# Optimization experiments

Hardware: AMD Instinct MI355X
Metric: run time of the kernel (lower is better)

Reference implementation:

```python
import jax, jax.numpy as jnp
import numpy as np
from jax import lax

B, L, S, D = 2, 8, 512, 256


def setup_inputs() -> dict:
    key = jax.random.key(0)
    ks = jax.random.split(key, 12)
    s = 1.0 / np.sqrt(D)
    return {
        "features": jax.random.normal(ks[0], (B, L, S, D), jnp.float32),
        "source_features": jax.random.normal(ks[1], (B, S, D), jnp.float32),
        "target_features": jax.random.normal(ks[2], (B, S, D), jnp.float32),
        # GRU params (torch layout: [3D, D] with gate order r, z, n)
        "W_ih": jax.random.uniform(ks[3], (3 * D, D), jnp.float32, -s, s),
        "W_hh": jax.random.uniform(ks[4], (3 * D, D), jnp.float32, -s, s),
        "b_ih": jax.random.uniform(ks[5], (3 * D,), jnp.float32, -s, s),
        "b_hh": jax.random.uniform(ks[6], (3 * D,), jnp.float32, -s, s),
        # causal_predictor: Linear(2D, D) -> ReLU -> Linear(D, D) -> Sigmoid
        "W1": jax.random.uniform(ks[7], (D, 2 * D), jnp.float32, -s, s),
        "b1": jax.random.uniform(ks[8], (D,), jnp.float32, -s, s),
        "W2": jax.random.uniform(ks[9], (D, D), jnp.float32, -s, s),
        "b2": jax.random.uniform(ks[10], (D,), jnp.float32, -s, s),
    }


def _gru(x, W_ih, W_hh, b_ih, b_hh):
    # x: [N, T, D] batch-first; returns all hidden states [N, T, D]
    N, T, d = x.shape
    gx = jnp.einsum('ntd,gd->ntg', x, W_ih) + b_ih  # [N, T, 3D]

    def step(h, gx_t):
        gh = h @ W_hh.T + b_hh
        r = jax.nn.sigmoid(gx_t[:, :d] + gh[:, :d])
        z = jax.nn.sigmoid(gx_t[:, d:2 * d] + gh[:, d:2 * d])
        n = jnp.tanh(gx_t[:, 2 * d:] + r * gh[:, 2 * d:])
        h_new = (1.0 - z) * n + z * h
        return h_new, h_new

    h0 = jnp.zeros((N, d), x.dtype)
    _, outs = lax.scan(step, h0, jnp.swapaxes(gx, 0, 1))  # [T, N, D]
    return jnp.swapaxes(outs, 0, 1)


def reference(features, source_features, target_features,
              W_ih, W_hh, b_ih, b_hh, W1, b1, W2, b2):
    b, l, s, d = features.shape
    fdim = jnp.float32(d)

    # --- track_feature_evolution, vectorized over seq positions ---
    # per-position GRU over the layer axis == one GRU over a B*S batch
    x = jnp.transpose(features, (0, 2, 1, 3)).reshape(b * s, l, d)
    evolution_out = _gru(x, W_ih, W_hh, b_ih, b_hh).reshape(b, s, l, d)

    prev = features[:, :-1]            # [B, L-1, S, D]
    nxt = features[:, 1:]
    eps = jnp.float32(1e-8)
    na = jnp.maximum(jnp.linalg.norm(prev, axis=-1), eps)
    nb = jnp.maximum(jnp.linalg.norm(nxt, axis=-1), eps)
    stability = (jnp.sum(prev * nxt, axis=-1) / (na * nb)).mean(axis=0)  # [L-1, S]

    act = jnp.sum((features > 0.1).astype(jnp.float32), axis=-1)  # [B, L, S]
    emergence = (act[:, 1:] - act[:, :-1]).mean(axis=0) / fdim    # [L-1, S]
    decay = (act[:, :-1] - act[:, 1:]).mean(axis=0) / fdim        # [L-1, S]

    # --- compute_causal_strength ---
    # combined[b,s,i,:D] = source[b,s,:]; combined[b,s,i,D+k] = target[b,s,i] (all k)
    # first Linear(2D->D) therefore splits into:  source @ W1a^T  +  target_i * sum_k W1b[:,k]
    W1a = W1[:, :d]                     # [D, D]
    wb = jnp.sum(W1[:, d:], axis=1)     # [D]
    A = jnp.einsum('bsd,od->bso', source_features, W1a) + b1  # [B, S, D]
    h = A[:, :, None, :] + target_features[:, :, :, None] * wb  # [B, S, D(i), D(o)]
    h = jax.nn.relu(h)
    out2 = jax.nn.sigmoid(jnp.einsum('bsio,po->bsip', h, W2) + b2)  # [B, S, D, D]
    causal_matrix = out2.mean(axis=(0, 1))  # [D, D]

    return stability, emergence, decay, causal_matrix, evolution_out
```

## Files before the change

kernel.cpp:

```cpp
#include <hip/hip_runtime.h>
#include <hip/hip_bf16.h>
#include <stdint.h>

typedef unsigned short u16;
typedef __bf16 v8bf __attribute__((ext_vector_type(8)));
typedef float f32x4 __attribute__((ext_vector_type(4)));

#define WS_WB    0u
#define WS_WIHB  4096u
#define WS_WHHB  397312u
#define WS_W2B   790528u
#define WS_A     921600u
#define WS_GX    2097152u
#define WS_PART  27262976u

#define OUT_STAB   0
#define OUT_EMER   3584
#define OUT_DECAY  7168
#define OUT_CAUSAL 10752
#define OUT_EVO    76288

__device__ __forceinline__ u16 f2bfu(float f){
    union { float f; uint32_t u; } v; v.f = f;
    uint32_t u = v.u;
    return (u16)((u + 0x7fffu + ((u >> 16) & 1u)) >> 16);
}
__device__ __forceinline__ float sigmoidf_fast(float x){
    float e = __builtin_amdgcn_exp2f(-1.4426950408889634f * x);
    return __builtin_amdgcn_rcpf(1.0f + e);
}
__device__ __forceinline__ float tanhf_fast(float x){
    float e = __builtin_amdgcn_exp2f(-2.8853900817779268f * x);
    return __builtin_amdgcn_rcpf(1.0f + e) * 2.0f - 1.0f;
}
__device__ __forceinline__ f32x4 mfma16(v8bf a, v8bf b, f32x4 c){
    return __builtin_amdgcn_mfma_f32_16x16x32_bf16(a, b, c, 0, 0, 0);
}
__device__ __forceinline__ v8bf cvt8(const float* p){
    float4 a = *(const float4*)p;
    float4 b = *(const float4*)(p + 4);
    v8bf r;
    r[0] = (__bf16)a.x; r[1] = (__bf16)a.y; r[2] = (__bf16)a.z; r[3] = (__bf16)a.w;
    r[4] = (__bf16)b.x; r[5] = (__bf16)b.y; r[6] = (__bf16)b.z; r[7] = (__bf16)b.w;
    return r;
}

__global__ void k_prep(const float* __restrict__ Wih, const float* __restrict__ Whh,
                       const float* __restrict__ W2,  const float* __restrict__ W1,
                       u16* __restrict__ wihb, u16* __restrict__ whhb,
                       u16* __restrict__ w2b, float* __restrict__ wb){
    int idx = blockIdx.x * 256 + threadIdx.x;
    if (idx < 196608) {
        wihb[idx] = f2bfu(Wih[idx]);
    } else if (idx < 393216) {
        int i = idx - 196608; whhb[i] = f2bfu(Whh[i]);
    } else if (idx < 458752) {
        int i = idx - 393216; w2b[i] = f2bfu(W2[i]);
    } else if (idx < 459008) {
        int o = idx - 458752;
        float s = 0.f;
        const float4* p = (const float4*)&W1[o * 512 + 256];
        for (int j = 0; j < 64; j++){
            float4 v = p[j];
            s += v.x + v.y + v.z + v.w;
        }
        wb[o] = s;
    }
}

__global__ __launch_bounds__(256) void k_Agemm(
        const float* __restrict__ src, const float* __restrict__ W1,
        const float* __restrict__ b1, float* __restrict__ A){
    const int bs0 = blockIdx.x * 16;
    const int tid = threadIdx.x, lane = tid & 63, w = tid >> 6;
    const int l15 = lane & 15, quad = lane >> 4;

    v8bf xa[8];
    for (int k = 0; k < 8; k++)
        xa[k] = cvt8(&src[(bs0 + l15) * 256 + k * 32 + quad * 8]);

    f32x4 acc[4];
    for (int nt = 0; nt < 4; nt++) acc[nt] = (f32x4){0.f, 0.f, 0.f, 0.f};
    for (int k = 0; k < 8; k++){
        int d0 = k * 32 + quad * 8;
        for (int nt = 0; nt < 4; nt++){
            int o = w * 64 + nt * 16 + l15;
            v8bf bfr = cvt8(&W1[o * 512 + d0]);
            acc[nt] = mfma16(xa[k], bfr, acc[nt]);
        }
    }
    for (int nt = 0; nt < 4; nt++){
        int o = w * 64 + nt * 16 + l15;
        float bb = b1[o];
        for (int r = 0; r < 4; r++)
            A[(bs0 + quad * 4 + r) * 256 + o] = acc[nt][r] + bb;
    }
}

__global__ void k_metrics(const float* __restrict__ feat, float* __restrict__ out){
    const int bid = blockIdx.x;
    const int l = bid >> 9, s = bid & 511;
    const int lane = threadIdx.x;
    float stab = 0.f, emer = 0.f;
    for (int b = 0; b < 2; b++){
        const float* p = feat + ((size_t)((b * 8 + l) * 512 + s)) * 256;
        const float* n = feat + ((size_t)((b * 8 + l + 1) * 512 + s)) * 256;
        float4 pv = *(const float4*)(p + lane * 4);
        float4 nv = *(const float4*)(n + lane * 4);
        float dot = pv.x * nv.x + pv.y * nv.y + pv.z * nv.z + pv.w * nv.w;
        float na2 = pv.x * pv.x + pv.y * pv.y + pv.z * pv.z + pv.w * pv.w;
        float nb2 = nv.x * nv.x + nv.y * nv.y + nv.z * nv.z + nv.w * nv.w;
        float ap = ((pv.x > 0.1f) ? 1.f : 0.f) + ((pv.y > 0.1f) ? 1.f : 0.f)
                 + ((pv.z > 0.1f) ? 1.f : 0.f) + ((pv.w > 0.1f) ? 1.f : 0.f);
        float an = ((nv.x > 0.1f) ? 1.f : 0.f) + ((nv.y > 0.1f) ? 1.f : 0.f)
                 + ((nv.z > 0.1f) ? 1.f : 0.f) + ((nv.w > 0.1f) ? 1.f : 0.f);
        for (int off = 32; off > 0; off >>= 1){
            dot += __shfl_xor(dot, off);
            na2 += __shfl_xor(na2, off);
            nb2 += __shfl_xor(nb2, off);
            ap  += __shfl_xor(ap,  off);
            an  += __shfl_xor(an,  off);
        }
        float na = fmaxf(__builtin_sqrtf(na2), 1e-8f);
        float nb = fmaxf(__builtin_sqrtf(nb2), 1e-8f);
        stab += dot / (na * nb);
        emer += (an - ap);
    }
    if (lane == 0){
        int o = l * 512 + s;
        float e = emer * 0.5f * (1.0f / 256.0f);
        out[OUT_STAB  + o] = stab * 0.5f;
        out[OUT_EMER  + o] = e;
        out[OUT_DECAY + o] = -e;
    }
}

__global__ __launch_bounds__(256, 2) void k_causal(
        const float* __restrict__ Aws, const float* __restrict__ wbws,
        const u16* __restrict__ w2b, const float* __restrict__ tgt,
        const float* __restrict__ b2, float* __restrict__ part){
    const int bid = blockIdx.x;
    const int chunk = bid >> 2, q = bid & 3;
    const int i0 = (q & 1) * 128, p0 = (q >> 1) * 128;
    const int tid = threadIdx.x, lane = tid & 63, w = tid >> 6;
    const int l15 = lane & 15, quad = lane >> 4;

    __shared__ u16  w2s[128 * 264];
    __shared__ float a_s[256];
    __shared__ float wb_s[256];
    __shared__ float t_s[128];

    {
        int r = tid >> 1, half = tid & 1;
        const uint4* gsrc = (const uint4*)&w2b[(p0 + r) * 256 + half * 128];
        uint4* ldst = (uint4*)&w2s[r * 264 + half * 128];
        for (int j = 0; j < 16; j++) ldst[j] = gsrc[j];
    }
    wb_s[tid] = wbws[tid];

    float bb[8];
    for (int nt = 0; nt < 8; nt++) bb[nt] = b2[p0 + nt * 16 + l15];

    f32x4 sig[2][8];
    for (int mt = 0; mt < 2; mt++) for (int nt = 0; nt < 8; nt++)
        sig[mt][nt] = (f32x4){0.f, 0.f, 0.f, 0.f};

    for (int ss = 0; ss < 8; ss++){
        const int bs = chunk * 8 + ss;
        __syncthreads();
        a_s[tid] = Aws[bs * 256 + tid];
        if (tid < 128) t_s[tid] = tgt[bs * 256 + i0 + tid];
        __syncthreads();

        float tv[2];
        for (int mt = 0; mt < 2; mt++) tv[mt] = t_s[w * 32 + mt * 16 + l15];

        f32x4 acc[2][8];
        for (int mt = 0; mt < 2; mt++) for (int nt = 0; nt < 8; nt++)
            acc[mt][nt] = (f32x4){0.f, 0.f, 0.f, 0.f};

        for (int k = 0; k < 8; k++){
            const int o0 = k * 32 + quad * 8;
            float4 a0 = *(const float4*)&a_s[o0];
            float4 a1 = *(const float4*)&a_s[o0 + 4];
            float4 w0 = *(const float4*)&wb_s[o0];
            float4 w1v = *(const float4*)&wb_s[o0 + 4];
            v8bf afr[2];
            for (int mt = 0; mt < 2; mt++){
                float t = tv[mt];
                float e0 = fmaxf(fmaf(t, w0.x,  a0.x), 0.f);
                float e1 = fmaxf(fmaf(t, w0.y,  a0.y), 0.f);
                float e2 = fmaxf(fmaf(t, w0.z,  a0.z), 0.f);
                float e3 = fmaxf(fmaf(t, w0.w,  a0.w), 0.f);
                float e4 = fmaxf(fmaf(t, w1v.x, a1.x), 0.f);
                float e5 = fmaxf(fmaf(t, w1v.y, a1.y), 0.f);
                float e6 = fmaxf(fmaf(t, w1v.z, a1.z), 0.f);
                float e7 = fmaxf(fmaf(t, w1v.w, a1.w), 0.f);
                v8bf af;
                af[0] = (__bf16)e0; af[1] = (__bf16)e1;
                af[2] = (__bf16)e2; af[3] = (__bf16)e3;
                af[4] = (__bf16)e4; af[5] = (__bf16)e5;
                af[6] = (__bf16)e6; af[7] = (__bf16)e7;
                afr[mt] = af;
            }
            for (int nt = 0; nt < 8; nt++){
                v8bf bfr = *(const v8bf*)&w2s[(nt * 16 + l15) * 264 + o0];
                acc[0][nt] = mfma16(afr[0], bfr, acc[0][nt]);
                acc[1][nt] = mfma16(afr[1], bfr, acc[1][nt]);
            }
        }
        for (int mt = 0; mt < 2; mt++)
            for (int nt = 0; nt < 8; nt++)
                for (int r = 0; r < 4; r++)
                    sig[mt][nt][r] += sigmoidf_fast(acc[mt][nt][r] + bb[nt]);
    }

    float* pp = part + (size_t)chunk * 65536;
    for (int mt = 0; mt < 2; mt++)
        for (int r = 0; r < 4; r++){
            int i = i0 + w * 32 + mt * 16 + quad * 4 + r;
            for (int nt = 0; nt < 8; nt++){
                int p = p0 + nt * 16 + l15;
                pp[i * 256 + p] = sig[mt][nt][r];
            }
        }
}

__global__ void k_creduce(const float* __restrict__ part, float* __restrict__ out){
    const int idx = blockIdx.x * 256 + threadIdx.x;
    float s = 0.f;
    for (int c = 0; c < 128; c++)
        s += part[(size_t)c * 65536 + idx];
    out[OUT_CAUSAL + idx] = s * (1.0f / 1024.0f);
}

__global__ __launch_bounds__(256) void k_gx(
        const float* __restrict__ feat, const u16* __restrict__ wihb,
        const float* __restrict__ bih, float* __restrict__ gxws){
    const int mb = blockIdx.x / 6, nb = blockIdx.x % 6;
    const int tid = threadIdx.x, lane = tid & 63, w = tid >> 6;
    const int l15 = lane & 15, quad = lane >> 4;

    __shared__ u16 blds[128 * 264];

    {
        int r = tid >> 1, half = tid & 1;
        const uint4* gsrc = (const uint4*)&wihb[(nb * 128 + r) * 256 + half * 128];
        uint4* ldst = (uint4*)&blds[r * 264 + half * 128];
        for (int j = 0; j < 16; j++) ldst[j] = gsrc[j];
    }

    v8bf af[2][8];
    for (int mt = 0; mt < 2; mt++){
        int r = mb * 128 + w * 32 + mt * 16 + l15;
        int n = r >> 3, t = r & 7;
        int b = n >> 9, s = n & 511;
        const float* xp = feat + ((size_t)((b * 8 + t) * 512 + s)) * 256;
        for (int kk = 0; kk < 8; kk++)
            af[mt][kk] = cvt8(xp + kk * 32 + quad * 8);
    }
    __syncthreads();

    f32x4 acc[2][8];
    for (int mt = 0; mt < 2; mt++) for (int nt = 0; nt < 8; nt++)
        acc[mt][nt] = (f32x4){0.f, 0.f, 0.f, 0.f};
    for (int kk = 0; kk < 8; kk++){
        int k0 = kk * 32 + quad * 8;
        for (int nt = 0; nt < 8; nt++){
            v8bf bf = *(const v8bf*)&blds[(nt * 16 + l15) * 264 + k0];
            acc[0][nt] = mfma16(af[0][kk], bf, acc[0][nt]);
            acc[1][nt] = mfma16(af[1][kk], bf, acc[1][nt]);
        }
    }
    for (int nt = 0; nt < 8; nt++){
        int g = nb * 128 + nt * 16 + l15;
        float bias = bih[g];
        for (int mt = 0; mt < 2; mt++)
            for (int rr = 0; rr < 4; rr++){
                int row = mb * 128 + w * 32 + mt * 16 + quad * 4 + rr;
                gxws[(size_t)row * 768 + g] = acc[mt][nt][rr] + bias;
            }
    }
}

__global__ __launch_bounds__(512) void k_gruseq(
        const float* __restrict__ gxws, const u16* __restrict__ whhb,
        const float* __restrict__ bhh, float* __restrict__ out){
    const int n0 = blockIdx.x * 16;
    const int tid = threadIdx.x, lane = tid & 63, wv = tid >> 6;
    const int l15 = lane & 15, quad = lane >> 4;
    const int g0 = wv * 96;

    __shared__ float h_lds[16 * 260];
    __shared__ float g_lds[16 * 776];

    v8bf wreg[3][8];
    for (int nt = 0; nt < 3; nt++)
        for (int k = 0; k < 8; k++)
            wreg[nt][k] = *(const v8bf*)&whhb[(g0 + nt * 16 + l15) * 256 + k * 32 + quad * 8];

    float bias[6];
    for (int nt = 0; nt < 6; nt++) bias[nt] = bhh[g0 + nt * 16 + l15];

    for (int e = tid; e < 16 * 260; e += 512) h_lds[e] = 0.f;

    const int seq = tid >> 5, d0 = (tid & 31) * 8;
    const float* gxbase = gxws + (size_t)(n0 + seq) * 8 * 768 + d0;
    float* evobase = out + OUT_EVO + (size_t)(n0 + seq) * 8 * 256 + d0;
    __syncthreads();

    for (int t = 0; t < 8; t++){
        v8bf ha[8];
        for (int k = 0; k < 8; k++)
            ha[k] = cvt8(&h_lds[l15 * 260 + k * 32 + quad * 8]);
        f32x4 acc[6];
        for (int nt = 0; nt < 6; nt++) acc[nt] = (f32x4){0.f, 0.f, 0.f, 0.f};
        for (int k = 0; k < 8; k++){
            int dk = k * 32 + quad * 8;
            acc[0] = mfma16(ha[k], wreg[0][k], acc[0]);
            acc[1] = mfma16(ha[k], wreg[1][k], acc[1]);
            acc[2] = mfma16(ha[k], wreg[2][k], acc[2]);
            for (int nt = 3; nt < 6; nt++){
                v8bf bf = *(const v8bf*)&whhb[(g0 + nt * 16 + l15) * 256 + dk];
                acc[nt] = mfma16(ha[k], bf, acc[nt]);
            }
        }
        for (int nt = 0; nt < 6; nt++){
            int g = g0 + nt * 16 + l15;
            for (int rr = 0; rr < 4; rr++)
                g_lds[(quad * 4 + rr) * 776 + g] = acc[nt][rr] + bias[nt];
        }
        const float* gxp = gxbase + (size_t)t * 768;
        float4 x0a = *(const float4*)(gxp);
        float4 x0b = *(const float4*)(gxp + 4);
        float4 x1a = *(const float4*)(gxp + 256);
        float4 x1b = *(const float4*)(gxp + 260);
        float4 x2a = *(const float4*)(gxp + 512);
        float4 x2b = *(const float4*)(gxp + 516);
        __syncthreads();
        {
            const float* gh = &g_lds[seq * 776];
            float* hp = &h_lds[seq * 260 + d0];
            float4 g0a = *(const float4*)&gh[d0];
            float4 g0b = *(const float4*)&gh[d0 + 4];
            float4 g1a = *(const float4*)&gh[256 + d0];
            float4 g1b = *(const float4*)&gh[260 + d0];
            float4 g2a = *(const float4*)&gh[512 + d0];
            float4 g2b = *(const float4*)&gh[516 + d0];
            float4 h0 = *(const float4*)hp;
            float4 h1 = *(const float4*)(hp + 4);
            float gxr[8] = {x0a.x, x0a.y, x0a.z, x0a.w, x0b.x, x0b.y, x0b.z, x0b.w};
            float gxz[8] = {x1a.x, x1a.y, x1a.z, x1a.w, x1b.x, x1b.y, x1b.z, x1b.w};
            float gxn[8] = {x2a.x, x2a.y, x2a.z, x2a.w, x2b.x, x2b.y, x2b.z, x2b.w};
            float ghr[8] = {g0a.x, g0a.y, g0a.z, g0a.w, g0b.x, g0b.y, g0b.z, g0b.w};
            float ghz[8] = {g1a.x, g1a.y, g1a.z, g1a.w, g1b.x, g1b.y, g1b.z, g1b.w};
            float ghn[8] = {g2a.x, g2a.y, g2a.z, g2a.w, g2b.x, g2b.y, g2b.z, g2b.w};
            float hold[8] = {h0.x, h0.y, h0.z, h0.w, h1.x, h1.y, h1.z, h1.w};
            float hn[8];
            #pragma unroll
            for (int j = 0; j < 8; j++){
                float r  = sigmoidf_fast(gxr[j] + ghr[j]);
                float z  = sigmoidf_fast(gxz[j] + ghz[j]);
                float nn = tanhf_fast(fmaf(r, ghn[j], gxn[j]));
                hn[j] = (1.f - z) * nn + z * hold[j];
            }
            float4 v0 = {hn[0], hn[1], hn[2], hn[3]};
            float4 v1 = {hn[4], hn[5], hn[6], hn[7]};
            *(float4*)hp       = v0;
            *(float4*)(hp + 4) = v1;
            float* ep = evobase + (size_t)t * 256;
            *(float4*)ep       = v0;
            *(float4*)(ep + 4) = v1;
        }
        __syncthreads();
    }
}

extern "C" void kernel_launch(void* const* d_in, const int* in_sizes, int n_in,
                              void* d_out, int out_size, void* d_ws, size_t ws_size,
                              hipStream_t stream){
    const float* feat = (const float*)d_in[0];
    const float* src  = (const float*)d_in[1];
    const float* tgt  = (const float*)d_in[2];
    const float* Wih  = (const float*)d_in[3];
    const float* Whh  = (const float*)d_in[4];
    const float* bih  = (const float*)d_in[5];
    const float* bhh  = (const float*)d_in[6];
    const float* W1   = (const float*)d_in[7];
    const float* b1   = (const float*)d_in[8];
    const float* W2   = (const float*)d_in[9];
    const float* b2   = (const float*)d_in[10];
    float* out = (float*)d_out;
    char* ws = (char*)d_ws;

    float* wb   = (float*)(ws + WS_WB);
    u16*   wihb = (u16*)(ws + WS_WIHB);
    u16*   whhb = (u16*)(ws + WS_WHHB);
    u16*   w2b  = (u16*)(ws + WS_W2B);
    float* Aws  = (float*)(ws + WS_A);
    float* gxws = (float*)(ws + WS_GX);
    float* part = (float*)(ws + WS_PART);

    k_prep   <<<1793, 256, 0, stream>>>(Wih, Whh, W2, W1, wihb, whhb, w2b, wb);
    k_gx     <<<384,  256, 0, stream>>>(feat, wihb, bih, gxws);
    k_Agemm  <<<64,   256, 0, stream>>>(src, W1, b1, Aws);
    k_metrics<<<3584,  64, 0, stream>>>(feat, out);
    k_causal <<<512,  256, 0, stream>>>(Aws, wb, w2b, tgt, b2, part);
    k_creduce<<<256,  256, 0, stream>>>(part, out);
    k_gruseq <<<64,   512, 0, stream>>>(gxws, whhb, bhh, out);
}
```

Baseline: 246.8 us.

## Consolidate launches into fused pre/final kernels and pre-convert features to bf16

Merges the A-GEMM, metrics and weight-prep kernels into one k_pre launch, which also converts the features tensor to bf16 in a workspace region that aliases the later partial-sum buffer. k_gx then reads bf16 features directly instead of converting on the fly. k_causal loads all 8 steps of A and target values into shared memory up front, removing two barriers per step, and reads wb from global memory. The causal reduction runs as extra blocks of the GRU sequence kernel so it can overlap with it. Together these cut the launch count from seven to four, at the cost of an extra full pass to write the bf16 copy of the features.

```diff
diff --git a/kernel.cpp b/kernel.cpp
--- a/kernel.cpp
+++ b/kernel.cpp
@@ -13,6 +13,7 @@
 #define WS_A     921600u
 #define WS_GX    2097152u
 #define WS_PART  27262976u
+#define WS_FEATB 27262976u
 
 #define OUT_STAB   0
 #define OUT_EMER   3584
@@ -45,93 +46,144 @@
     return r;
 }
 
-__global__ void k_prep(const float* __restrict__ Wih, const float* __restrict__ Whh,
-                       const float* __restrict__ W2,  const float* __restrict__ W1,
-                       u16* __restrict__ wihb, u16* __restrict__ whhb,
-                       u16* __restrict__ w2b, float* __restrict__ wb){
-    int idx = blockIdx.x * 256 + threadIdx.x;
-    if (idx < 196608) {
-        wihb[idx] = f2bfu(Wih[idx]);
-    } else if (idx < 393216) {
-        int i = idx - 196608; whhb[i] = f2bfu(Whh[i]);
-    } else if (idx < 458752) {
-        int i = idx - 393216; w2b[i] = f2bfu(W2[i]);
-    } else if (idx < 459008) {
-        int o = idx - 458752;
-        float s = 0.f;
-        const float4* p = (const float4*)&W1[o * 512 + 256];
-        for (int j = 0; j < 64; j++){
-            float4 v = p[j];
-            s += v.x + v.y + v.z + v.w;
-        }
-        wb[o] = s;
-    }
-}
-
-__global__ __launch_bounds__(256) void k_Agemm(
-        const float* __restrict__ src, const float* __restrict__ W1,
-        const float* __restrict__ b1, float* __restrict__ A){
-    const int bs0 = blockIdx.x * 16;
+__global__ __launch_bounds__(256) void k_pre(
+        const float* __restrict__ feat, const float* __restrict__ src,
+        const float* __restrict__ Wih,  const float* __restrict__ Whh,
+        const float* __restrict__ W1,   const float* __restrict__ b1,
+        const float* __restrict__ W2,
+        u16* __restrict__ wihb, u16* __restrict__ whhb, u16* __restrict__ w2b,
+        float* __restrict__ wb, u16* __restrict__ featb,
+        float* __restrict__ A, float* __restrict__ out){
+    const int bid = blockIdx.x, tid = threadIdx.x;
+    if (bid < 64){
+        const int bs0 = bid * 16;
+        const int lane = tid & 63, w = tid >> 6;
+        const int l15 = lane & 15, quad = lane >> 4;
+        v8bf xa[8];
+        for (int k = 0; k < 8; k++)
+            xa[k] = cvt8(&src[(bs0 + l15) * 256 + k * 32 + quad * 8]);
+        f32x4 acc[4];
+        for (int nt = 0; nt < 4; nt++) acc[nt] = (f32x4){0.f, 0.f, 0.f, 0.f};
+        for (int k = 0; k < 8; k++){
+            int d0 = k * 32 + quad * 8;
+            for (int nt = 0; nt < 4; nt++){
+                int o = w * 64 + nt * 16 + l15;
+                v8bf bfr = cvt8(&W1[o * 512 + d0]);
+                acc[nt] = mfma16(xa[k], bfr, acc[nt]);
+            }
+        }
+        for (int nt = 0; nt < 4; nt++){
+            int o = w * 64 + nt * 16 + l15;
+            float bb = b1[o];
+            for (int r = 0; r < 4; r++)
+                A[(bs0 + quad * 4 + r) * 256 + o] = acc[nt][r] + bb;
+        }
+    } else if (bid < 960){
+        const int pair = (bid - 64) * 4 + (tid >> 6);
+        const int l = pair >> 9, s = pair & 511;
+        const int lane = tid & 63;
+        float stab = 0.f, emer = 0.f;
+        for (int b = 0; b < 2; b++){
+            const float* p = feat + ((size_t)((b * 8 + l) * 512 + s)) * 256;
+            const float* n = feat + ((size_t)((b * 8 + l + 1) * 512 + s)) * 256;
+            float4 pv = *(const float4*)(p + lane * 4);
+            float4 nv = *(const float4*)(n + lane * 4);
+            float dot = pv.x * nv.x + pv.y * nv.y + pv.z * nv.z + pv.w * nv.w;
+            float na2 = pv.x * pv.x + pv.y * pv.y + pv.z * pv.z + pv.w * pv.w;
+            float nb2 = nv.x * nv.x + nv.y * nv.y + nv.z * nv.z + nv.w * nv.w;
+            float ap = ((pv.x > 0.1f) ? 1.f : 0.f) + ((pv.y > 0.1f) ? 1.f : 0.f)
+                     + ((pv.z > 0.1f) ? 1.f : 0.f) + ((pv.w > 0.1f) ? 1.f : 0.f);
+            float an = ((nv.x > 0.1f) ? 1.f : 0.f) + ((nv.y > 0.1f) ? 1.f : 0.f)
+                     + ((nv.z > 0.1f) ? 1.f : 0.f) + ((nv.w > 0.1f) ? 1.f : 0.f);
+            for (int off = 32; off > 0; off >>= 1){
+                dot += __shfl_xor(dot, off);
+                na2 += __shfl_xor(na2, off);
+                nb2 += __shfl_xor(nb2, off);
+                ap  += __shfl_xor(ap,  off);
+                an  += __shfl_xor(an,  off);
+            }
+            float na = fmaxf(__builtin_sqrtf(na2), 1e-8f);
+            float nb = fmaxf(__builtin_sqrtf(nb2), 1e-8f);
+            stab += dot / (na * nb);
+            emer += (an - ap);
+        }
+        if (lane == 0){
+            int o = l * 512 + s;
+            float e = emer * 0.5f * (1.0f / 256.0f);
+            out[OUT_STAB  + o] = stab * 0.5f;
+            out[OUT_EMER  + o] = e;
+            out[OUT_DECAY + o] = -e;
+        }
+    } else {
+        int idx = (bid - 960) * 256 + tid;
+        if (idx < 196608) {
+            wihb[idx] = f2bfu(Wih[idx]);
+        } else if (idx < 393216) {
+            int i = idx - 196608; whhb[i] = f2bfu(Whh[i]);
+        } else if (idx < 458752) {
+            int i = idx - 393216; w2b[i] = f2bfu(W2[i]);
+        } else if (idx < 459008) {
+            int o = idx - 458752;
+            float s = 0.f;
+            const float4* p = (const float4*)&W1[o * 512 + 256];
+            for (int j = 0; j < 64; j++){
+                float4 v = p[j];
+                s += v.x + v.y + v.z + v.w;
+            }
+            wb[o] = s;
+        } else {
+            int i = idx - 459008;
+            featb[i] = f2bfu(feat[i]);
+        }
+    }
+}
+
+__global__ __launch_bounds__(256) void k_gx(
+        const u16* __restrict__ featb, const u16* __restrict__ wihb,
+        const float* __restrict__ bih, float* __restrict__ gxws){
+    const int mb = blockIdx.x / 6, nb = blockIdx.x % 6;
     const int tid = threadIdx.x, lane = tid & 63, w = tid >> 6;
     const int l15 = lane & 15, quad = lane >> 4;
 
-    v8bf xa[8];
-    for (int k = 0; k < 8; k++)
-        xa[k] = cvt8(&src[(bs0 + l15) * 256 + k * 32 + quad * 8]);
-
-    f32x4 acc[4];
-    for (int nt = 0; nt < 4; nt++) acc[nt] = (f32x4){0.f, 0.f, 0.f, 0.f};
-    for (int k = 0; k < 8; k++){
-        int d0 = k * 32 + quad * 8;
-        for (int nt = 0; nt < 4; nt++){
-            int o = w * 64 + nt * 16 + l15;
-            v8bf bfr = cvt8(&W1[o * 512 + d0]);
-            acc[nt] = mfma16(xa[k], bfr, acc[nt]);
-        }
-    }
-    for (int nt = 0; nt < 4; nt++){
-        int o = w * 64 + nt * 16 + l15;
-        float bb = b1[o];
-        for (int r = 0; r < 4; r++)
-            A[(bs0 + quad * 4 + r) * 256 + o] = acc[nt][r] + bb;
-    }
-}
-
-__global__ void k_metrics(const float* __restrict__ feat, float* __restrict__ out){
-    const int bid = blockIdx.x;
-    const int l = bid >> 9, s = bid & 511;
-    const int lane = threadIdx.x;
-    float stab = 0.f, emer = 0.f;
-    for (int b = 0; b < 2; b++){
-        const float* p = feat + ((size_t)((b * 8 + l) * 512 + s)) * 256;
-        const float* n = feat + ((size_t)((b * 8 + l + 1) * 512 + s)) * 256;
-        float4 pv = *(const float4*)(p + lane * 4);
-        float4 nv = *(const float4*)(n + lane * 4);
-        float dot = pv.x * nv.x + pv.y * nv.y + pv.z * nv.z + pv.w * nv.w;
-        float na2 = pv.x * pv.x + pv.y * pv.y + pv.z * pv.z + pv.w * pv.w;
-        float nb2 = nv.x * nv.x + nv.y * nv.y + nv.z * nv.z + nv.w * nv.w;
-        float ap = ((pv.x > 0.1f) ? 1.f : 0.f) + ((pv.y > 0.1f) ? 1.f : 0.f)
-                 + ((pv.z > 0.1f) ? 1.f : 0.f) + ((pv.w > 0.1f) ? 1.f : 0.f);
-        float an = ((nv.x > 0.1f) ? 1.f : 0.f) + ((nv.y > 0.1f) ? 1.f : 0.f)
-                 + ((nv.z > 0.1f) ? 1.f : 0.f) + ((nv.w > 0.1f) ? 1.f : 0.f);
-        for (int off = 32; off > 0; off >>= 1){
-            dot += __shfl_xor(dot, off);
-            na2 += __shfl_xor(na2, off);
-            nb2 += __shfl_xor(nb2, off);
-            ap  += __shfl_xor(ap,  off);
-            an  += __shfl_xor(an,  off);
-        }
-        float na = fmaxf(__builtin_sqrtf(na2), 1e-8f);
-        float nb = fmaxf(__builtin_sqrtf(nb2), 1e-8f);
-        stab += dot / (na * nb);
-        emer += (an - ap);
-    }
-    if (lane == 0){
-        int o = l * 512 + s;
-        float e = emer * 0.5f * (1.0f / 256.0f);
-        out[OUT_STAB  + o] = stab * 0.5f;
-        out[OUT_EMER  + o] = e;
-        out[OUT_DECAY + o] = -e;
+    __shared__ u16 blds[128 * 264];
+
+    {
+        int r = tid >> 1, half = tid & 1;
+        const uint4* gsrc = (const uint4*)&wihb[(nb * 128 + r) * 256 + half * 128];
+        uint4* ldst = (uint4*)&blds[r * 264 + half * 128];
+        for (int j = 0; j < 16; j++) ldst[j] = gsrc[j];
+    }
+
+    v8bf af[2][8];
+    for (int mt = 0; mt < 2; mt++){
+        int r = mb * 128 + w * 32 + mt * 16 + l15;
+        int n = r >> 3, t = r & 7;
+        int b = n >> 9, s = n & 511;
+        const u16* xp = featb + ((size_t)((b * 8 + t) * 512 + s)) * 256;
+        for (int kk = 0; kk < 8; kk++)
+            af[mt][kk] = *(const v8bf*)(xp + kk * 32 + quad * 8);
+    }
+    __syncthreads();
+
+    f32x4 acc[2][8];
+    for (int mt = 0; mt < 2; mt++) for (int nt = 0; nt < 8; nt++)
+        acc[mt][nt] = (f32x4){0.f, 0.f, 0.f, 0.f};
+    for (int kk = 0; kk < 8; kk++){
+        int k0 = kk * 32 + quad * 8;
+        for (int nt = 0; nt < 8; nt++){
+            v8bf bf = *(const v8bf*)&blds[(nt * 16 + l15) * 264 + k0];
+            acc[0][nt] = mfma16(af[0][kk], bf, acc[0][nt]);
+            acc[1][nt] = mfma16(af[1][kk], bf, acc[1][nt]);
+        }
+    }
+    for (int nt = 0; nt < 8; nt++){
+        int g = nb * 128 + nt * 16 + l15;
+        float bias = bih[g];
+        for (int mt = 0; mt < 2; mt++)
+            for (int rr = 0; rr < 4; rr++){
+                int row = mb * 128 + w * 32 + mt * 16 + quad * 4 + rr;
+                gxws[(size_t)row * 768 + g] = acc[mt][nt][rr] + bias;
+            }
     }
 }
 
@@ -146,9 +198,8 @@
     const int l15 = lane & 15, quad = lane >> 4;
 
     __shared__ u16  w2s[128 * 264];
-    __shared__ float a_s[256];
-    __shared__ float wb_s[256];
-    __shared__ float t_s[128];
+    __shared__ float a_all[8 * 256];
+    __shared__ float t_all[8 * 128];
 
     {
         int r = tid >> 1, half = tid & 1;
@@ -156,7 +207,17 @@
         uint4* ldst = (uint4*)&w2s[r * 264 + half * 128];
         for (int j = 0; j < 16; j++) ldst[j] = gsrc[j];
     }
-    wb_s[tid] = wbws[tid];
+    {
+        const float4* src4 = (const float4*)&Aws[chunk * 8 * 256];
+        float4* dst4 = (float4*)a_all;
+        dst4[tid]       = src4[tid];
+        dst4[tid + 256] = src4[tid + 256];
+    }
+    {
+        int ss = tid >> 5, j4 = tid & 31;
+        float4 v = *(const float4*)&tgt[(chunk * 8 + ss) * 256 + i0 + j4 * 4];
+        *(float4*)&t_all[ss * 128 + j4 * 4] = v;
+    }
 
     float bb[8];
     for (int nt = 0; nt < 8; nt++) bb[nt] = b2[p0 + nt * 16 + l15];
@@ -165,15 +226,11 @@
     for (int mt = 0; mt < 2; mt++) for (int nt = 0; nt < 8; nt++)
         sig[mt][nt] = (f32x4){0.f, 0.f, 0.f, 0.f};
 
+    __syncthreads();
+
     for (int ss = 0; ss < 8; ss++){
-        const int bs = chunk * 8 + ss;
-        __syncthreads();
-        a_s[tid] = Aws[bs * 256 + tid];
-        if (tid < 128) t_s[tid] = tgt[bs * 256 + i0 + tid];
-        __syncthreads();
-
-        float tv[2];
-        for (int mt = 0; mt < 2; mt++) tv[mt] = t_s[w * 32 + mt * 16 + l15];
+        float tv0 = t_all[ss * 128 + w * 32 + l15];
+        float tv1 = t_all[ss * 128 + w * 32 + 16 + l15];
 
         f32x4 acc[2][8];
         for (int mt = 0; mt < 2; mt++) for (int nt = 0; nt < 8; nt++)
@@ -181,32 +238,37 @@
 
         for (int k = 0; k < 8; k++){
             const int o0 = k * 32 + quad * 8;
-            float4 a0 = *(const float4*)&a_s[o0];
-            float4 a1 = *(const float4*)&a_s[o0 + 4];
-            float4 w0 = *(const float4*)&wb_s[o0];
-            float4 w1v = *(const float4*)&wb_s[o0 + 4];
-            v8bf afr[2];
-            for (int mt = 0; mt < 2; mt++){
-                float t = tv[mt];
-                float e0 = fmaxf(fmaf(t, w0.x,  a0.x), 0.f);
-                float e1 = fmaxf(fmaf(t, w0.y,  a0.y), 0.f);
-                float e2 = fmaxf(fmaf(t, w0.z,  a0.z), 0.f);
-                float e3 = fmaxf(fmaf(t, w0.w,  a0.w), 0.f);
-                float e4 = fmaxf(fmaf(t, w1v.x, a1.x), 0.f);
-                float e5 = fmaxf(fmaf(t, w1v.y, a1.y), 0.f);
-                float e6 = fmaxf(fmaf(t, w1v.z, a1.z), 0.f);
-                float e7 = fmaxf(fmaf(t, w1v.w, a1.w), 0.f);
-                v8bf af;
-                af[0] = (__bf16)e0; af[1] = (__bf16)e1;
-                af[2] = (__bf16)e2; af[3] = (__bf16)e3;
-                af[4] = (__bf16)e4; af[5] = (__bf16)e5;
-                af[6] = (__bf16)e6; af[7] = (__bf16)e7;
-                afr[mt] = af;
+            float4 a0  = *(const float4*)&a_all[ss * 256 + o0];
+            float4 a1  = *(const float4*)&a_all[ss * 256 + o0 + 4];
+            float4 w0  = *(const float4*)&wbws[o0];
+            float4 w1v = *(const float4*)&wbws[o0 + 4];
+            v8bf afr0, afr1;
+            {
+                float t = tv0;
+                afr0[0] = (__bf16)fmaxf(fmaf(t, w0.x,  a0.x), 0.f);
+                afr0[1] = (__bf16)fmaxf(fmaf(t, w0.y,  a0.y), 0.f);
+                afr0[2] = (__bf16)fmaxf(fmaf(t, w0.z,  a0.z), 0.f);
+                afr0[3] = (__bf16)fmaxf(fmaf(t, w0.w,  a0.w), 0.f);
+                afr0[4] = (__bf16)fmaxf(fmaf(t, w1v.x, a1.x), 0.f);
+                afr0[5] = (__bf16)fmaxf(fmaf(t, w1v.y, a1.y), 0.f);
+                afr0[6] = (__bf16)fmaxf(fmaf(t, w1v.z, a1.z), 0.f);
+                afr0[7] = (__bf16)fmaxf(fmaf(t, w1v.w, a1.w), 0.f);
+            }
+            {
+                float t = tv1;
+                afr1[0] = (__bf16)fmaxf(fmaf(t, w0.x,  a0.x), 0.f);
+                afr1[1] = (__bf16)fmaxf(fmaf(t, w0.y,  a0.y), 0.f);
+                afr1[2] = (__bf16)fmaxf(fmaf(t, w0.z,  a0.z), 0.f);
+                afr1[3] = (__bf16)fmaxf(fmaf(t, w0.w,  a0.w), 0.f);
+                afr1[4] = (__bf16)fmaxf(fmaf(t, w1v.x, a1.x), 0.f);
+                afr1[5] = (__bf16)fmaxf(fmaf(t, w1v.y, a1.y), 0.f);
+                afr1[6] = (__bf16)fmaxf(fmaf(t, w1v.z, a1.z), 0.f);
+                afr1[7] = (__bf16)fmaxf(fmaf(t, w1v.w, a1.w), 0.f);
             }
             for (int nt = 0; nt < 8; nt++){
                 v8bf bfr = *(const v8bf*)&w2s[(nt * 16 + l15) * 264 + o0];
-                acc[0][nt] = mfma16(afr[0], bfr, acc[0][nt]);
-                acc[1][nt] = mfma16(afr[1], bfr, acc[1][nt]);
+                acc[0][nt] = mfma16(afr0, bfr, acc[0][nt]);
+                acc[1][nt] = mfma16(afr1, bfr, acc[1][nt]);
             }
         }
         for (int mt = 0; mt < 2; mt++)
@@ -226,66 +288,18 @@
         }
 }
 
-__global__ void k_creduce(const float* __restrict__ part, float* __restrict__ out){
-    const int idx = blockIdx.x * 256 + threadIdx.x;
-    float s = 0.f;
-    for (int c = 0; c < 128; c++)
-        s += part[(size_t)c * 65536 + idx];
-    out[OUT_CAUSAL + idx] = s * (1.0f / 1024.0f);
-}
-
-__global__ __launch_bounds__(256) void k_gx(
-        const float* __restrict__ feat, const u16* __restrict__ wihb,
-        const float* __restrict__ bih, float* __restrict__ gxws){
-    const int mb = blockIdx.x / 6, nb = blockIdx.x % 6;
-    const int tid = threadIdx.x, lane = tid & 63, w = tid >> 6;
-    const int l15 = lane & 15, quad = lane >> 4;
-
-    __shared__ u16 blds[128 * 264];
-
-    {
-        int r = tid >> 1, half = tid & 1;
-        const uint4* gsrc = (const uint4*)&wihb[(nb * 128 + r) * 256 + half * 128];
-        uint4* ldst = (uint4*)&blds[r * 264 + half * 128];
-        for (int j = 0; j < 16; j++) ldst[j] = gsrc[j];
-    }
-
-    v8bf af[2][8];
-    for (int mt = 0; mt < 2; mt++){
-        int r = mb * 128 + w * 32 + mt * 16 + l15;
-        int n = r >> 3, t = r & 7;
-        int b = n >> 9, s = n & 511;
-        const float* xp = feat + ((size_t)((b * 8 + t) * 512 + s)) * 256;
-        for (int kk = 0; kk < 8; kk++)
-            af[mt][kk] = cvt8(xp + kk * 32 + quad * 8);
-    }
-    __syncthreads();
-
-    f32x4 acc[2][8];
-    for (int mt = 0; mt < 2; mt++) for (int nt = 0; nt < 8; nt++)
-        acc[mt][nt] = (f32x4){0.f, 0.f, 0.f, 0.f};
-    for (int kk = 0; kk < 8; kk++){
-        int k0 = kk * 32 + quad * 8;
-        for (int nt = 0; nt < 8; nt++){
-            v8bf bf = *(const v8bf*)&blds[(nt * 16 + l15) * 264 + k0];
-            acc[0][nt] = mfma16(af[0][kk], bf, acc[0][nt]);
-            acc[1][nt] = mfma16(af[1][kk], bf, acc[1][nt]);
-        }
-    }
-    for (int nt = 0; nt < 8; nt++){
-        int g = nb * 128 + nt * 16 + l15;
-        float bias = bih[g];
-        for (int mt = 0; mt < 2; mt++)
-            for (int rr = 0; rr < 4; rr++){
-                int row = mb * 128 + w * 32 + mt * 16 + quad * 4 + rr;
-                gxws[(size_t)row * 768 + g] = acc[mt][nt][rr] + bias;
-            }
-    }
-}
-
-__global__ __launch_bounds__(512) void k_gruseq(
+__global__ __launch_bounds__(512) void k_final(
         const float* __restrict__ gxws, const u16* __restrict__ whhb,
-        const float* __restrict__ bhh, float* __restrict__ out){
+        const float* __restrict__ bhh, const float* __restrict__ part,
+        float* __restrict__ out){
+    if (blockIdx.x >= 64){
+        const int idx = (blockIdx.x - 64) * 512 + threadIdx.x;
+        float s = 0.f;
+        for (int c = 0; c < 128; c++)
+            s += part[(size_t)c * 65536 + idx];
+        out[OUT_CAUSAL + idx] = s * (1.0f / 1024.0f);
+        return;
+    }
     const int n0 = blockIdx.x * 16;
     const int tid = threadIdx.x, lane = tid & 63, wv = tid >> 6;
     const int l15 = lane & 15, quad = lane >> 4;
@@ -400,12 +414,11 @@
     float* Aws  = (float*)(ws + WS_A);
     float* gxws = (float*)(ws + WS_GX);
     float* part = (float*)(ws + WS_PART);
-
-    k_prep   <<<1793, 256, 0, stream>>>(Wih, Whh, W2, W1, wihb, whhb, w2b, wb);
-    k_gx     <<<384,  256, 0, stream>>>(feat, wihb, bih, gxws);
-    k_Agemm  <<<64,   256, 0, stream>>>(src, W1, b1, Aws);
-    k_metrics<<<3584,  64, 0, stream>>>(feat, out);
-    k_causal <<<512,  256, 0, stream>>>(Aws, wb, w2b, tgt, b2, part);
-    k_creduce<<<256,  256, 0, stream>>>(part, out);
-    k_gruseq <<<64,   512, 0, stream>>>(gxws, whhb, bhh, out);
-}
+    u16*   featb= (u16*)(ws + WS_FEATB);
+
+    k_pre   <<<10945, 256, 0, stream>>>(feat, src, Wih, Whh, W1, b1, W2,
+                                        wihb, whhb, w2b, wb, featb, Aws, out);
+    k_gx    <<<384,   256, 0, stream>>>(featb, wihb, bih, gxws);
+    k_causal<<<512,   256, 0, stream>>>(Aws, wb, w2b, tgt, b2, part);
+    k_final <<<192,   512, 0, stream>>>(gxws, whhb, bhh, part, out);
+}
```

New measurement: 383.9 us. 55.6% more time.
